# Performance work log

Measured on AMD Instinct MI355X. Metric: run time of the kernel, lower is better.

## Reference

```python
import jax, jax.numpy as jnp
import numpy as np
import math

B, T, C, H, S = 2, 2048, 1024, 16, 16
HD = C // H
EPS = 1e-5


def setup_inputs() -> dict:
    key = jax.random.key(0)
    ks = jax.random.split(key, 20)
    sc = 1.0 / math.sqrt(C)
    inp = {
        "x": jax.random.normal(ks[0], (B, T, C), jnp.float32),
        # A_log_fwd: log(arange(1..S)) repeated over dim (as in __init__)
        "A_log": jnp.log(jnp.tile(jnp.arange(1, S + 1, dtype=jnp.float32), (C, 1))),
        # Linear weights stored (in, out); apply as x @ W + b
        "Wd": jax.random.normal(ks[1], (C, C), jnp.float32) * sc,
        "bd": jnp.full((C,), -3.0, jnp.float32),
        "WB": jax.random.normal(ks[2], (C, S), jnp.float32) * sc,
        "WC": jax.random.normal(ks[3], (C, S), jnp.float32) * sc,
        "Wq": jax.random.normal(ks[4], (C, C), jnp.float32) * sc,
        "bq": jnp.zeros((C,), jnp.float32),
        "Wk": jax.random.normal(ks[5], (C, C), jnp.float32) * sc,
        "bk": jnp.zeros((C,), jnp.float32),
        "Wv": jax.random.normal(ks[6], (C, C), jnp.float32) * sc,
        "bv": jnp.zeros((C,), jnp.float32),
        "Wx": jax.random.normal(ks[7], (C, C), jnp.float32) * sc,
        "bx": jnp.zeros((C,), jnp.float32),
        "Wo": jax.random.normal(ks[8], (C, C), jnp.float32) * sc,
        "bo": jnp.zeros((C,), jnp.float32),
        "ln_g": jnp.ones((C,), jnp.float32),
        "ln_b": jnp.zeros((C,), jnp.float32),
        "temp": jnp.full((1, H, 1, 1), 0.5, jnp.float32),
    }
    return inp


def _forward(x, A_log, Wd, bd, WB, WC, Wq, bq, Wk, bk, Wv, bv, Wx, bx, Wo, bo, ln_g, ln_b, temp):
    x_base = x @ Wx + bx                      # (B,T,C)
    delta = jax.nn.softplus(x @ Wd + bd)      # (B,T,C)
    B_mat = x @ WB                            # (B,T,S)
    C_mat = x @ WC                            # (B,T,S)
    A = -jnp.exp(A_log)                       # (C,S)

    def scan_fn(h, inp):
        xb_t, d_t, B_t, C_t = inp             # (B,C),(B,C),(B,S),(B,S)
        bar_A = jnp.exp(d_t[..., None] * A)   # (B,C,S)
        h = bar_A * h + (d_t * xb_t)[..., None] * B_t[:, None, :]
        y = jnp.einsum('bcs,bs->bc', h, C_t)
        return h, y

    h0 = jnp.zeros((B, C, S), x.dtype)
    xs = (jnp.swapaxes(x_base, 0, 1), jnp.swapaxes(delta, 0, 1),
          jnp.swapaxes(B_mat, 0, 1), jnp.swapaxes(C_mat, 0, 1))
    _, ys = jax.lax.scan(scan_fn, h0, xs)
    out_fwd = jnp.swapaxes(ys, 0, 1)          # (B,T,C)

    # LayerNorm(x_base + out_fwd)
    hyb = x_base + out_fwd
    mu = hyb.mean(-1, keepdims=True)
    var = hyb.var(-1, keepdims=True)
    hybrid = (hyb - mu) * jax.lax.rsqrt(var + EPS) * ln_g + ln_b

    def heads(W, b):
        return (hybrid @ W + b).reshape(B, T, H, HD).transpose(0, 2, 1, 3)

    Q, K, V = heads(Wq, bq), heads(Wk, bk), heads(Wv, bv)
    scores = jnp.einsum('bhqd,bhkd->bhqk', Q, K) / math.sqrt(HD)
    scores = scores * jax.nn.softplus(temp)
    mask = jnp.tril(jnp.ones((T, T), bool))
    scores = jnp.where(mask[None, None], scores, -jnp.inf)
    attn = jax.nn.softmax(scores, axis=-1)
    out = jnp.einsum('bhqk,bhkd->bhqd', attn, V).transpose(0, 2, 1, 3).reshape(B, T, C)
    return out @ Wo + bo


def reference(x, A_log, Wd, bd, WB, WC, Wq, bq, Wk, bk, Wv, bv, Wx, bx, Wo, bo, ln_g, ln_b, temp):
    return _forward(x, A_log, Wd, bd, WB, WC, Wq, bq, Wk, bk, Wv, bv, Wx, bx, Wo, bo, ln_g, ln_b, temp)
```

## Files before the change

kernel.cpp:

```cpp
#include <hip/hip_runtime.h>
#include <math.h>

#define B_  2
#define T_  2048
#define C_  1024
#define H_  16
#define S_  16
#define HD_ 64
#define NCH 32
#define CHL 64

typedef short  short8  __attribute__((ext_vector_type(8)));
typedef unsigned short ushort8 __attribute__((ext_vector_type(8)));
typedef unsigned short ushort4v __attribute__((ext_vector_type(4)));
typedef float  f32x4   __attribute__((ext_vector_type(4)));

__device__ __forceinline__ float softplus_f(float v) {
    return fmaxf(v, 0.f) + log1pf(__expf(-fabsf(v)));
}

__device__ __forceinline__ unsigned short f2bf(float x) {
    unsigned u = __float_as_uint(x);
    u += 0x7fffu + ((u >> 16) & 1u);
    return (unsigned short)(u >> 16);
}

__device__ __forceinline__ void gload16(const unsigned short* g,
                                        unsigned short* l)
{
    __builtin_amdgcn_global_load_lds(
        (const __attribute__((address_space(1))) unsigned int*)g,
        (__attribute__((address_space(3))) unsigned int*)l, 16, 0, 0);
}

__global__ __launch_bounds__(256) void cast_bf16(const float* __restrict__ in,
                                                 unsigned short* __restrict__ out,
                                                 int n4)
{
    int i = blockIdx.x * 256 + threadIdx.x;
    if (i >= n4) return;
    float4 v = ((const float4*)in)[i];
    ushort4v o = {f2bf(v.x), f2bf(v.y), f2bf(v.z), f2bf(v.w)};
    ((ushort4v*)out)[i] = o;
}

__device__ __forceinline__ void wtrans_body(const float* __restrict__ W,
                                            unsigned short* __restrict__ WT,
                                            int bx, int by, int tid)
{
    __shared__ float t[32][33];
    const int n0 = bx * 32, k0 = by * 32;
    const int tx = tid & 31, ty = tid >> 5;
#pragma unroll
    for (int p = 0; p < 4; ++p)
        t[ty + p * 8][tx] = W[(size_t)(k0 + ty + p * 8) * C_ + n0 + tx];
    __syncthreads();
#pragma unroll
    for (int p = 0; p < 4; ++p)
        WT[(size_t)(n0 + ty + p * 8) * C_ + k0 + tx] = f2bf(t[tx][ty + p * 8]);
}

__global__ __launch_bounds__(256) void wtrans(const float* __restrict__ W,
                                              unsigned short* __restrict__ WT)
{
    wtrans_body(W, WT, blockIdx.x, blockIdx.y, threadIdx.x);
}

__global__ __launch_bounds__(256) void wtrans_multi(
    const float* __restrict__ Wx, const float* __restrict__ Wd,
    const float* __restrict__ Wq, const float* __restrict__ Wk,
    const float* __restrict__ Wv,
    unsigned short* __restrict__ Astack, unsigned short* __restrict__ Wqkv)
{
    const float* src;
    unsigned short* dst;
    switch (blockIdx.z) {
        case 0: src = Wx; dst = Astack; break;
        case 1: src = Wd; dst = Astack + (size_t)1024 * 1024; break;
        case 2: src = Wq; dst = Wqkv; break;
        case 3: src = Wk; dst = Wqkv + (size_t)1024 * 1024; break;
        default: src = Wv; dst = Wqkv + (size_t)2048 * 1024; break;
    }
    wtrans_body(src, dst, blockIdx.x, blockIdx.y, threadIdx.x);
}

__global__ __launch_bounds__(256) void prep_misc(
    const float* __restrict__ WB, const float* __restrict__ WC,
    const float* __restrict__ bx, const float* __restrict__ bd,
    const float* __restrict__ bq, const float* __restrict__ bk,
    const float* __restrict__ bv,
    unsigned short* __restrict__ Astack, float* __restrict__ biasPD,
    float* __restrict__ biasQKV)
{
    int gid = blockIdx.x * 256 + threadIdx.x;
    if (gid < 32768) {
        int w = gid >> 14, rem = gid & 16383;
        int s = rem >> 10, k = rem & 1023;
        const float* src = w ? WC : WB;
        Astack[(size_t)(2048 + w * 16 + s) * 1024 + k] = f2bf(src[k * 16 + s]);
    } else {
        int id = gid - 32768;
        if (id < 2176) {
            biasPD[id] = id < 1024 ? bx[id] : (id < 2048 ? bd[id - 1024] : 0.f);
        } else {
            int id2 = id - 2176;
            if (id2 < 3072)
                biasQKV[id2] = id2 < 1024 ? bq[id2]
                             : (id2 < 2048 ? bk[id2 - 1024] : bv[id2 - 2048]);
        }
    }
}

__global__ __launch_bounds__(256) void gemm_mfma(
    const unsigned short* __restrict__ A, const unsigned short* __restrict__ Bm,
    const float* __restrict__ bias,
    void* __restrict__ outv,
    int M, int N, int K, int lda)
{
    __shared__ __align__(16) unsigned short As[4][4096];
    __shared__ __align__(16) unsigned short Bs[4][4096];

    const int tid = threadIdx.x;
    const int w = tid >> 6, lane = tid & 63;
    const int lq = lane & 15, lg = lane >> 4;
    const int wm = w >> 1, wn = w & 1;
    const int mBase = blockIdx.y * 128, nBase = blockIdx.x * 128;

    const int c0 = tid, c1 = tid + 256;
    const int rA0 = ((c0 >> 6) << 4) + (c0 & 15), kO0 = ((c0 >> 4) & 3) << 3;
    const int rA1 = ((c1 >> 6) << 4) + (c1 & 15), kO1 = ((c1 >> 4) & 3) << 3;

    const int wL0 = w * 512;
    const int wL1 = 2048 + w * 512;

    f32x4 acc[4][4];
#pragma unroll
    for (int i = 0; i < 4; ++i)
#pragma unroll
        for (int j = 0; j < 4; ++j) acc[i][j] = (f32x4){0.f, 0.f, 0.f, 0.f};

    const unsigned short* ga0 = A  + (size_t)(mBase + rA0) * lda + kO0;
    const unsigned short* ga1 = A  + (size_t)(mBase + rA1) * lda + kO1;
    const unsigned short* gb0 = Bm + (size_t)(nBase + rA0) * lda + kO0;
    const unsigned short* gb1 = Bm + (size_t)(nBase + rA1) * lda + kO1;

    #define STAGE(bufv, k0v)                               \
        do {                                               \
            gload16(ga0 + (k0v), &As[bufv][wL0]);          \
            gload16(ga1 + (k0v), &As[bufv][wL1]);          \
            gload16(gb0 + (k0v), &Bs[bufv][wL0]);          \
            gload16(gb1 + (k0v), &Bs[bufv][wL1]);          \
        } while (0)
    #define COMPUTE(bufv)                                                       \
        do {                                                                    \
            short8 a[4], b[4];                                                  \
            _Pragma("unroll")                                                   \
            for (int i = 0; i < 4; ++i)                                         \
                a[i] = *(const short8*)&As[bufv][((wm * 4 + i) * 64 + lg * 16 + lq) * 8]; \
            _Pragma("unroll")                                                   \
            for (int j = 0; j < 4; ++j)                                         \
                b[j] = *(const short8*)&Bs[bufv][((wn * 4 + j) * 64 + lg * 16 + lq) * 8]; \
            _Pragma("unroll")                                                   \
            for (int i = 0; i < 4; ++i)                                         \
                _Pragma("unroll")                                               \
                for (int j = 0; j < 4; ++j)                                     \
                    acc[i][j] = __builtin_amdgcn_mfma_f32_16x16x32_bf16(        \
                        a[i], b[j], acc[i][j], 0, 0, 0);                        \
        } while (0)
    #define WAITV4() asm volatile("s_waitcnt vmcnt(4)" ::: "memory")
    #define WAITV0() asm volatile("s_waitcnt vmcnt(0)" ::: "memory")
    #define LGKM0()  asm volatile("s_waitcnt lgkmcnt(0)" ::: "memory")
    #define STEP(cbuf, kt)                                          \
        do {                                                        \
            if ((kt) + 32 < K) WAITV4(); else WAITV0();             \
            LGKM0();                                                \
            __builtin_amdgcn_s_barrier();                           \
            if ((kt) + 64 < K) STAGE(((cbuf) + 2) & 3, (kt) + 64);  \
            COMPUTE(cbuf);                                          \
        } while (0)

    STAGE(0, 0);
    STAGE(1, 32);

    for (int k0 = 0; k0 < K; k0 += 128) {
        STEP(0, k0);
        STEP(1, k0 + 32);
        STEP(2, k0 + 64);
        STEP(3, k0 + 96);
    }
    #undef STAGE
    #undef COMPUTE
    #undef WAITV4
    #undef WAITV0
    #undef LGKM0
    #undef STEP

    float* O = (float*)outv;
#pragma unroll
    for (int j = 0; j < 4; ++j) {
        int Cg = nBase + wn * 64 + j * 16 + lq;
        float bb = bias[Cg];
#pragma unroll
        for (int i = 0; i < 4; ++i) {
            int Rb = mBase + wm * 64 + i * 16 + lg * 4;
#pragma unroll
            for (int r = 0; r < 4; ++r)
                O[(size_t)(Rb + r) * N + Cg] = acc[i][j][r] + bb;
        }
    }
}

__global__ __launch_bounds__(512, 2) void gemm_projT(
    const unsigned short* __restrict__ A, const unsigned short* __restrict__ Bm,
    const float* __restrict__ bias,
    float* __restrict__ xbaseT, float* __restrict__ deltaT,
    float* __restrict__ BmT, float* __restrict__ CmT,
    int K, int lda)
{
    __shared__ __align__(16) unsigned short AS[2][2][4096];
    __shared__ __align__(16) unsigned short BS[2][2][8192];

    const int tid = threadIdx.x;
    const int w = tid >> 6, lane = tid & 63;
    const int lq = lane & 15, lg = lane >> 4;
    const int wm = w >> 2, wn = w & 3;
    const int mBase = blockIdx.y * 128, nBase = blockIdx.x * 256;

    const int rA = ((tid >> 6) << 4) | (tid & 15);
    const int kA = ((tid >> 4) & 3) << 3;
    const unsigned short* gA = A + (size_t)(mBase + rA) * lda + kA;
    const int eA = tid * 8;
    const int c0 = tid, c1 = tid + 512;
    const int rB0 = ((c0 >> 6) << 4) | (c0 & 15), kB0 = ((c0 >> 4) & 3) << 3;
    const int rB1 = ((c1 >> 6) << 4) | (c1 & 15), kB1 = ((c1 >> 4) & 3) << 3;
    const unsigned short* gB0 = Bm + (size_t)(nBase + rB0) * lda + kB0;
    const unsigned short* gB1 = Bm + (size_t)(nBase + rB1) * lda + kB1;

    f32x4 acc[4][4];
#pragma unroll
    for (int i = 0; i < 4; ++i)
#pragma unroll
        for (int j = 0; j < 4; ++j) acc[i][j] = (f32x4){0.f, 0.f, 0.f, 0.f};

    #define STG(buf_, half_, kb_)                                             \
        do {                                                                  \
            gload16(gA  + (kb_) + (half_) * 32, &AS[buf_][half_][eA]);        \
            gload16(gB0 + (kb_) + (half_) * 32, &BS[buf_][half_][c0 * 8]);    \
            gload16(gB1 + (kb_) + (half_) * 32, &BS[buf_][half_][c1 * 8]);    \
        } while (0)
    #define WAITV6() asm volatile("s_waitcnt vmcnt(6)" ::: "memory")
    #define WAITV3() asm volatile("s_waitcnt vmcnt(3)" ::: "memory")
    #define WAITV0() asm volatile("s_waitcnt vmcnt(0)" ::: "memory")

    #define PHASE(buf_, half_, STAGE_STMT, GATE_STMT)                         \
        do {                                                                  \
            short8 a_[4], b_[4];                                              \
            _Pragma("unroll")                                                 \
            for (int i = 0; i < 4; ++i)                                       \
                a_[i] = *(const short8*)&AS[buf_][half_]                      \
                    [((wm * 4 + i) * 64 + lg * 16 + lq) * 8];                 \
            _Pragma("unroll")                                                 \
            for (int j = 0; j < 4; ++j)                                       \
                b_[j] = *(const short8*)&BS[buf_][half_]                      \
                    [((wn * 4 + j) * 64 + lg * 16 + lq) * 8];                 \
            STAGE_STMT;                                                       \
            __builtin_amdgcn_s_barrier();                                     \
            asm volatile("s_waitcnt lgkmcnt(0)" ::: "memory");                \
            __builtin_amdgcn_s_setprio(1);                                    \
            _Pragma("unroll")                                                 \
            for (int i = 0; i < 4; ++i)                                       \
                _Pragma("unroll")                                             \
                for (int j = 0; j < 4; ++j)                                   \
                    acc[i][j] = __builtin_amdgcn_mfma_f32_16x16x32_bf16(      \
                        a_[i], b_[j], acc[i][j], 0, 0, 0);                    \
            __builtin_amdgcn_s_setprio(0);                                    \
            GATE_STMT;                                                        \
            __builtin_amdgcn_s_barrier();                                     \
        } while (0)

    STG(0, 0, 0);
    STG(0, 1, 0);
    STG(1, 0, 64);
    WAITV6();
    __builtin_amdgcn_s_barrier();

    const int NT = K >> 6;
    for (int kt = 0; kt < NT; ++kt) {
        const int buf = kt & 1, nbuf = buf ^ 1;
        const int kb1 = (kt + 1) << 6, kb2 = (kt + 2) << 6;
        PHASE(buf, 0, { if (kt + 1 < NT) STG(nbuf, 1, kb1); },
              { if (kt < NT - 1) WAITV6(); else WAITV3(); });
        PHASE(buf, 1, { if (kt + 2 < NT) STG(buf, 0, kb2); },
              { if (kt < NT - 2) WAITV6();
                else if (kt == NT - 2) WAITV3(); else WAITV0(); });
    }
    #undef STG
    #undef WAITV6
    #undef WAITV3
    #undef WAITV0
    #undef PHASE

#pragma unroll
    for (int i = 0; i < 4; ++i) {
        int Rb = mBase + wm * 64 + i * 16 + lg * 4;
        if (Rb >= 2080) continue;
        float bb[4];
#pragma unroll
        for (int r = 0; r < 4; ++r) bb[r] = bias[Rb + r];
#pragma unroll
        for (int j = 0; j < 4; ++j) {
            int Cg = nBase + wn * 64 + j * 16 + lq;
            int b = Cg >> 11, t = Cg & (T_ - 1);
#pragma unroll
            for (int r = 0; r < 4; ++r) {
                int R = Rb + r;
                float v = acc[i][j][r] + bb[r];
                if (Rb < 1024) {
                    xbaseT[((size_t)b * C_ + R) * T_ + t] = v;
                } else if (Rb < 2048) {
                    deltaT[((size_t)b * C_ + (R - 1024)) * T_ + t] =
                        softplus_f(v);
                } else if (Rb < 2064) {
                    BmT[((size_t)b * S_ + (R - 2048)) * T_ + t] = v;
                } else {
                    CmT[((size_t)b * S_ + (R - 2064)) * T_ + t] = v;
                }
            }
        }
    }
}

__global__ __launch_bounds__(512, 2) void gemm_mfma256(
    const unsigned short* __restrict__ A, const unsigned short* __restrict__ Bm,
    const float* __restrict__ bias,
    void* __restrict__ outv, void* __restrict__ out2,
    void* __restrict__ out3,
    int M, int N, int K, int lda)
{
    __shared__ __align__(16) unsigned short AS[2][2][8192];
    __shared__ __align__(16) unsigned short BS[2][2][8192];

    const int tid = threadIdx.x;
    const int w = tid >> 6, lane = tid & 63;
    const int lq = lane & 15, lg = lane >> 4;
    const int wm = w >> 2, wn = w & 3;
    const int mBase = blockIdx.y * 256, nBase = blockIdx.x * 256;

    const int c0 = tid, c1 = tid + 512;
    const int r0 = ((c0 >> 6) << 4) | (c0 & 15), k0l = ((c0 >> 4) & 3) << 3;
    const int r1 = ((c1 >> 6) << 4) | (c1 & 15), k1l = ((c1 >> 4) & 3) << 3;
    const unsigned short* gA0 = A  + (size_t)(mBase + r0) * lda + k0l;
    const unsigned short* gA1 = A  + (size_t)(mBase + r1) * lda + k1l;
    const unsigned short* gB0 = Bm + (size_t)(nBase + r0) * lda + k0l;
    const unsigned short* gB1 = Bm + (size_t)(nBase + r1) * lda + k1l;

    f32x4 acc[8][4];
#pragma unroll
    for (int i = 0; i < 8; ++i)
#pragma unroll
        for (int j = 0; j < 4; ++j) acc[i][j] = (f32x4){0.f, 0.f, 0.f, 0.f};

    #define STG_A(buf_, half_, kb_)                                           \
        do {                                                                  \
            gload16(gA0 + (kb_) + (half_) * 32, &AS[buf_][half_][c0 * 8]);    \
            gload16(gA1 + (kb_) + (half_) * 32, &AS[buf_][half_][c1 * 8]);    \
        } while (0)
    #define STG_B(buf_, half_, kb_)                                           \
        do {                                                                  \
            gload16(gB0 + (kb_) + (half_) * 32, &BS[buf_][half_][c0 * 8]);    \
            gload16(gB1 + (kb_) + (half_) * 32, &BS[buf_][half_][c1 * 8]);    \
        } while (0)
    #define WAITV8() asm volatile("s_waitcnt vmcnt(8)" ::: "memory")
    #define WAITV4() asm volatile("s_waitcnt vmcnt(4)" ::: "memory")
    #define WAITV0() asm volatile("s_waitcnt vmcnt(0)" ::: "memory")

    #define PHASE(buf_, half_, qi_, STAGE_STMT, GATE_STMT)                    \
        do {                                                                  \
            short8 a_[4];                                                     \
            _Pragma("unroll")                                                 \
            for (int i = 0; i < 4; ++i)                                       \
                a_[i] = *(const short8*)&AS[buf_][half_]                      \
                    [((wm * 8 + (qi_) * 4 + i) * 64 + lg * 16 + lq) * 8];     \
            if ((qi_) == 0) {                                                 \
                _Pragma("unroll")                                             \
                for (int j = 0; j < 4; ++j)                                   \
                    bfr[j] = *(const short8*)&BS[buf_][half_]                 \
                        [((wn * 4 + j) * 64 + lg * 16 + lq) * 8];             \
            }                                                                 \
            STAGE_STMT;                                                       \
            __builtin_amdgcn_s_barrier();                                     \
            asm volatile("s_waitcnt lgkmcnt(0)" ::: "memory");                \
            __builtin_amdgcn_s_setprio(1);                                    \
            _Pragma("unroll")                                                 \
            for (int i = 0; i < 4; ++i)                                       \
                _Pragma("unroll")                                             \
                for (int j = 0; j < 4; ++j)                                   \
                    acc[(qi_) * 4 + i][j] =                                   \
                        __builtin_amdgcn_mfma_f32_16x16x32_bf16(              \
                            a_[i], bfr[j], acc[(qi_) * 4 + i][j], 0, 0, 0);   \
            __builtin_amdgcn_s_setprio(0);                                    \
            GATE_STMT;                                                        \
            __builtin_amdgcn_s_barrier();                                     \
        } while (0)

    STG_A(0, 0, 0);
    STG_B(0, 0, 0);
    STG_A(0, 1, 0);
    STG_B(0, 1, 0);
    STG_A(1, 0, 64);
    STG_B(1, 0, 64);
    WAITV8();
    __builtin_amdgcn_s_barrier();

    const int NT = K >> 6;
    for (int kt = 0; kt < NT; ++kt) {
        const int buf = kt & 1, nbuf = buf ^ 1;
        const int kb1 = (kt + 1) << 6, kb2 = (kt + 2) << 6;
        short8 bfr[4];
        PHASE(buf, 0, 0, { if (kt + 1 < NT) STG_A(nbuf, 1, kb1); }, {});
        PHASE(buf, 0, 1, { if (kt + 1 < NT) STG_B(nbuf, 1, kb1); },
              { if (kt < NT - 1) WAITV8(); else WAITV0(); });
        PHASE(buf, 1, 0, { if (kt + 2 < NT) STG_A(buf, 0, kb2); }, {});
        PHASE(buf, 1, 1, { if (kt + 2 < NT) STG_B(buf, 0, kb2); },
              { if (kt < NT - 2) WAITV8();
                else if (kt == NT - 2) WAITV4(); });
    }
    #undef STG_A
    #undef STG_B
    #undef WAITV8
    #undef WAITV4
    #undef WAITV0
    #undef PHASE

    unsigned short* Qb  = (unsigned short*)outv;
    unsigned short* Kb  = (unsigned short*)out2;
    unsigned short* VTb = (unsigned short*)out3;
#pragma unroll
    for (int j = 0; j < 4; ++j) {
        int Cg = nBase + wn * 64 + j * 16 + lq;
        int reg = Cg >> 10, c = Cg & 1023;
        int h = c >> 6, hd = c & 63;
        float bb = bias[Cg];
#pragma unroll
        for (int i = 0; i < 8; ++i) {
            int Rb = mBase + wm * 128 + i * 16 + lg * 4;
#pragma unroll
            for (int r = 0; r < 4; ++r) {
                int R = Rb + r, b = R >> 11, t = R & (T_ - 1);
                unsigned short o = f2bf(acc[i][j][r] + bb);
                if (reg == 0)
                    Qb[(((size_t)(b * H_ + h) * T_ + t) * HD_) + hd] = o;
                else if (reg == 1)
                    Kb[(((size_t)(b * H_ + h) * T_ + t) * HD_) + hd] = o;
                else
                    VTb[(((size_t)(b * H_ + h) * HD_ + hd) * T_) + t] = o;
            }
        }
    }
}

__global__ __launch_bounds__(256) void scan_partial(
    const float* __restrict__ xbaseT, const float* __restrict__ deltaT,
    const float* __restrict__ BmT, const float* __restrict__ A_log,
    float4* __restrict__ Pbuf, float4* __restrict__ Lbuf)
{
    const int tid = threadIdx.x;
    const int s4 = tid & 3;
    const int cm = tid >> 2;
    const int cg = blockIdx.x & 15;
    const int k  = (blockIdx.x >> 4) & (NCH - 1);
    const int b  = blockIdx.x >> 9;
    const int c  = cg * 64 + cm;

    float a[4];
#pragma unroll
    for (int j = 0; j < 4; ++j)
        a[j] = -__expf(A_log[c * S_ + s4 * 4 + j]);

    const int tb = k * CHL;
    const float* dp = deltaT + ((size_t)b * C_ + c) * T_ + tb;
    const float* xp = xbaseT + ((size_t)b * C_ + c) * T_ + tb;
    const float* bp = BmT + ((size_t)(b * S_ + s4 * 4)) * T_ + tb;

    float L[4] = {0.f, 0.f, 0.f, 0.f};
    float sumd = 0.f;
    for (int t0 = 0; t0 < CHL; t0 += 4) {
        float4 d4 = *(const float4*)&dp[t0];
        float4 x4 = *(const float4*)&xp[t0];
        float dv[4] = {d4.x, d4.y, d4.z, d4.w};
        float xv[4] = {x4.x, x4.y, x4.z, x4.w};
        float bv[4][4];
#pragma unroll
        for (int j = 0; j < 4; ++j) {
            float4 b4 = *(const float4*)&bp[(size_t)j * T_ + t0];
            bv[j][0] = b4.x; bv[j][1] = b4.y; bv[j][2] = b4.z; bv[j][3] = b4.w;
        }
#pragma unroll
        for (int q = 0; q < 4; ++q) {
            float u = dv[q] * xv[q];
            sumd += dv[q];
#pragma unroll
            for (int j = 0; j < 4; ++j)
                L[j] = fmaf(__expf(dv[q] * a[j]), L[j], u * bv[j][q]);
        }
    }
    int gid = blockIdx.x * 256 + tid;
    float4 P4 = {__expf(a[0] * sumd), __expf(a[1] * sumd),
                 __expf(a[2] * sumd), __expf(a[3] * sumd)};
    float4 L4 = {L[0], L[1], L[2], L[3]};
    Pbuf[gid] = P4;
    Lbuf[gid] = L4;
}

__global__ __launch_bounds__(256) void scan_final(
    const float* __restrict__ xbaseT, const float* __restrict__ deltaT,
    const float* __restrict__ BmT, const float* __restrict__ CmT,
    const float* __restrict__ A_log, const float4* __restrict__ Pbuf,
    const float4* __restrict__ Lbuf, float* __restrict__ hyb)
{
    const int tid = threadIdx.x;
    const int s4 = tid & 3;
    const int cm = tid >> 2;
    const int cg = blockIdx.x & 15;
    const int k  = (blockIdx.x >> 4) & (NCH - 1);
    const int b  = blockIdx.x >> 9;
    const int c  = cg * 64 + cm;

    float h[4] = {0.f, 0.f, 0.f, 0.f};
    for (int k2 = 0; k2 < k; ++k2) {
        int gid2 = (((b * NCH + k2) << 4) + cg) * 256 + tid;
        float4 P4 = Pbuf[gid2];
        float4 L4 = Lbuf[gid2];
        h[0] = fmaf(P4.x, h[0], L4.x);
        h[1] = fmaf(P4.y, h[1], L4.y);
        h[2] = fmaf(P4.z, h[2], L4.z);
        h[3] = fmaf(P4.w, h[3], L4.w);
    }

    float a[4];
#pragma unroll
    for (int j = 0; j < 4; ++j)
        a[j] = -__expf(A_log[c * S_ + s4 * 4 + j]);

    const int tb = k * CHL;
    const float* dp = deltaT + ((size_t)b * C_ + c) * T_ + tb;
    const float* xp = xbaseT + ((size_t)b * C_ + c) * T_ + tb;
    const float* bp = BmT + ((size_t)(b * S_ + s4 * 4)) * T_ + tb;
    const float* cp = CmT + ((size_t)(b * S_ + s4 * 4)) * T_ + tb;
    float* hp = hyb + ((size_t)b * T_ + tb) * C_ + c;

    for (int t0 = 0; t0 < CHL; t0 += 4) {
        float4 d4 = *(const float4*)&dp[t0];
        float4 x4 = *(const float4*)&xp[t0];
        float dv[4] = {d4.x, d4.y, d4.z, d4.w};
        float xv[4] = {x4.x, x4.y, x4.z, x4.w};
        float bv[4][4], cv[4][4];
#pragma unroll
        for (int j = 0; j < 4; ++j) {
            float4 b4 = *(const float4*)&bp[(size_t)j * T_ + t0];
            float4 c4 = *(const float4*)&cp[(size_t)j * T_ + t0];
            bv[j][0] = b4.x; bv[j][1] = b4.y; bv[j][2] = b4.z; bv[j][3] = b4.w;
            cv[j][0] = c4.x; cv[j][1] = c4.y; cv[j][2] = c4.z; cv[j][3] = c4.w;
        }
#pragma unroll
        for (int q = 0; q < 4; ++q) {
            float u = dv[q] * xv[q];
#pragma unroll
            for (int j = 0; j < 4; ++j)
                h[j] = fmaf(__expf(dv[q] * a[j]), h[j], u * bv[j][q]);
            float y = h[0] * cv[0][q];
            y = fmaf(h[1], cv[1][q], y);
            y = fmaf(h[2], cv[2][q], y);
            y = fmaf(h[3], cv[3][q], y);
            y += __shfl_xor(y, 1, 64);
            y += __shfl_xor(y, 2, 64);
            if (s4 == 0) hp[(size_t)(t0 + q) * C_] = xv[q] + y;
        }
    }
}

__global__ __launch_bounds__(256) void layernorm_kernel(
    const float* __restrict__ in, const float* __restrict__ g,
    const float* __restrict__ beta, unsigned short* __restrict__ out)
{
    const int row = blockIdx.x;
    const float* rp = in + (size_t)row * C_;
    const int c = threadIdx.x * 4;
    float4 v = *(const float4*)&rp[c];
    float sum = v.x + v.y + v.z + v.w;
    float sq = v.x * v.x + v.y * v.y + v.z * v.z + v.w * v.w;
#pragma unroll
    for (int off = 1; off < 64; off <<= 1) {
        sum += __shfl_xor(sum, off, 64);
        sq += __shfl_xor(sq, off, 64);
    }
    __shared__ float sS[4], sQ[4];
    int wave = threadIdx.x >> 6, lane = threadIdx.x & 63;
    if (lane == 0) { sS[wave] = sum; sQ[wave] = sq; }
    __syncthreads();
    sum = sS[0] + sS[1] + sS[2] + sS[3];
    sq = sQ[0] + sQ[1] + sQ[2] + sQ[3];
    const float mu = sum * (1.f / C_);
    const float var = sq * (1.f / C_) - mu * mu;
    const float rstd = rsqrtf(var + 1e-5f);
    float4 gg = *(const float4*)&g[c];
    float4 bb = *(const float4*)&beta[c];
    ushort4v o;
    o.x = f2bf((v.x - mu) * rstd * gg.x + bb.x);
    o.y = f2bf((v.y - mu) * rstd * gg.y + bb.y);
    o.z = f2bf((v.z - mu) * rstd * gg.z + bb.z);
    o.w = f2bf((v.w - mu) * rstd * gg.w + bb.w);
    *(ushort4v*)&out[(size_t)row * C_ + c] = o;
}

#define BKT 128
#define KP  72
#define VP  136
__global__ __launch_bounds__(256) void attn_mfma(
    const unsigned short* __restrict__ Q, const unsigned short* __restrict__ K,
    const unsigned short* __restrict__ VT, const float* __restrict__ temp,
    unsigned short* __restrict__ out)
{
    __shared__ __align__(16) unsigned short Ks[BKT * KP];
    __shared__ __align__(16) unsigned short Vs[80 * VP];
    __shared__ __align__(16) unsigned short Ps[64 * VP];

    const int tid = threadIdx.x;
    const int w = tid >> 6, lane = tid & 63;
    const int lq = lane & 15, lg = lane >> 4;
    const int p  = blockIdx.x & 15;
    const int bh = blockIdx.x >> 4;
    const int b = bh >> 4, h = bh & 15;

    const float scale = softplus_f(temp[h]) * 0.125f;
    const unsigned short* Qp = Q + (size_t)bh * T_ * HD_;
    const unsigned short* Kp = K + (size_t)bh * T_ * HD_;
    const unsigned short* Vp = VT + (size_t)bh * HD_ * T_;

    {
        int r = 64 + (tid >> 4), o = (tid & 15) * 8;
        ushort8 ones = {0x3f80, 0x3f80, 0x3f80, 0x3f80,
                        0x3f80, 0x3f80, 0x3f80, 0x3f80};
        *(ushort8*)&Vs[r * VP + o] = ones;
    }

    ushort8 kreg[4], vreg[4];
    #define LOADKV(jtv)                                                        \
        do {                                                                   \
            int kb = (jtv) * BKT;                                              \
            _Pragma("unroll")                                                  \
            for (int q2 = 0; q2 < 4; ++q2) {                                   \
                int c = tid + q2 * 256;                                        \
                kreg[q2] = *(const ushort8*)&Kp[(size_t)(kb + (c >> 3)) * HD_  \
                                                + (c & 7) * 8];                \
                vreg[q2] = *(const ushort8*)&Vp[(size_t)(c >> 4) * T_ + kb     \
                                                + (c & 15) * 8];               \
            }                                                                  \
        } while (0)

    for (int half = 0; half < 2; ++half) {
        const int qi = half ? p : (31 - p);
        const int qbase = qi * 64;
        const int nT = (qbase + 64 + BKT - 1) / BKT;

        short8 qf[2];
#pragma unroll
        for (int s = 0; s < 2; ++s)
            qf[s] = *(const short8*)&Qp[(size_t)(qbase + w * 16 + lq) * HD_
                                        + s * 32 + lg * 8];
        LOADKV(0);

        float m_i[4];
        f32x4 o[5];
#pragma unroll
        for (int r = 0; r < 4; ++r) m_i[r] = -INFINITY;
#pragma unroll
        for (int j = 0; j < 5; ++j) o[j] = (f32x4){0.f, 0.f, 0.f, 0.f};

        for (int jt = 0; jt < nT; ++jt) {
            const int kbase = jt * BKT;
            const bool last = (jt == nT - 1);
            __syncthreads();
#pragma unroll
            for (int q2 = 0; q2 < 4; ++q2) {
                int c = tid + q2 * 256;
                *(ushort8*)&Ks[(c >> 3) * KP + (c & 7) * 8] = kreg[q2];
                *(ushort8*)&Vs[(c >> 4) * VP + (c & 15) * 8] = vreg[q2];
            }
            __syncthreads();
            if (jt + 1 < nT) LOADKV(jt + 1);

            f32x4 sacc[8];
#pragma unroll
            for (int j = 0; j < 8; ++j) sacc[j] = (f32x4){0.f, 0.f, 0.f, 0.f};
#pragma unroll
            for (int s = 0; s < 2; ++s) {
#pragma unroll
                for (int j = 0; j < 8; ++j) {
                    short8 kf = *(const short8*)&Ks[(j * 16 + lq) * KP
                                                    + s * 32 + lg * 8];
                    sacc[j] = __builtin_amdgcn_mfma_f32_16x16x32_bf16(
                        qf[s], kf, sacc[j], 0, 0, 0);
                }
            }

#pragma unroll
            for (int r = 0; r < 4; ++r) {
                int qrow = qbase + w * 16 + lg * 4 + r;
                float sv[8];
#pragma unroll
                for (int j = 0; j < 8; ++j) {
                    sv[j] = sacc[j][r] * scale;
                    if (last && (kbase + j * 16 + lq > qrow)) sv[j] = -INFINITY;
                }
                float mx = sv[0];
#pragma unroll
                for (int j = 1; j < 8; ++j) mx = fmaxf(mx, sv[j]);
                mx = fmaxf(mx, __shfl_xor(mx, 1, 64));
                mx = fmaxf(mx, __shfl_xor(mx, 2, 64));
                mx = fmaxf(mx, __shfl_xor(mx, 4, 64));
                mx = fmaxf(mx, __shfl_xor(mx, 8, 64));
                float mnew = fmaxf(m_i[r], mx);
                float alpha = __expf(m_i[r] - mnew);
                m_i[r] = mnew;
#pragma unroll
                for (int j = 0; j < 5; ++j) o[j][r] *= alpha;
#pragma unroll
                for (int j = 0; j < 8; ++j)
                    Ps[(w * 16 + lg * 4 + r) * VP + j * 16 + lq] =
                        f2bf(__expf(sv[j] - mnew));
            }

#pragma unroll
            for (int s2 = 0; s2 < 4; ++s2) {
                short8 pf = *(const short8*)&Ps[(w * 16 + lq) * VP
                                                + s2 * 32 + lg * 8];
#pragma unroll
                for (int j = 0; j < 5; ++j) {
                    short8 vf = *(const short8*)&Vs[(j * 16 + lq) * VP
                                                    + s2 * 32 + lg * 8];
                    o[j] = __builtin_amdgcn_mfma_f32_16x16x32_bf16(
                        pf, vf, o[j], 0, 0, 0);
                }
            }
        }

#pragma unroll
        for (int r = 0; r < 4; ++r) {
            float inv = 1.f / o[4][r];
            int qrow = qbase + w * 16 + lg * 4 + r;
#pragma unroll
            for (int j = 0; j < 4; ++j)
                out[((size_t)(b * T_ + qrow)) * C_ + h * 64 + j * 16 + lq] =
                    f2bf(o[j][r] * inv);
        }
    }
    #undef LOADKV
}

extern "C" void kernel_launch(void* const* d_in, const int* in_sizes, int n_in,
                              void* d_out, int out_size, void* d_ws, size_t ws_size,
                              hipStream_t stream)
{
    const float* x     = (const float*)d_in[0];
    const float* A_log = (const float*)d_in[1];
    const float* Wd    = (const float*)d_in[2];
    const float* bd    = (const float*)d_in[3];
    const float* WB    = (const float*)d_in[4];
    const float* WC    = (const float*)d_in[5];
    const float* Wq    = (const float*)d_in[6];
    const float* bq    = (const float*)d_in[7];
    const float* Wk    = (const float*)d_in[8];
    const float* bk    = (const float*)d_in[9];
    const float* Wv    = (const float*)d_in[10];
    const float* bv    = (const float*)d_in[11];
    const float* Wx    = (const float*)d_in[12];
    const float* bx    = (const float*)d_in[13];
    const float* Wo    = (const float*)d_in[14];
    const float* bo    = (const float*)d_in[15];
    const float* ln_g  = (const float*)d_in[16];
    const float* ln_b  = (const float*)d_in[17];
    const float* temp  = (const float*)d_in[18];

    char* wsb = (char*)d_ws;
    const size_t MB = 1024 * 1024;
    const size_t HMB = 512 * 1024;
    unsigned short* xb      = (unsigned short*)(wsb);
    float4* Pbuf            = (float4*)(wsb);
    float4* Lbuf            = (float4*)(wsb + 4 * MB);
    unsigned short* hybrid  = (unsigned short*)(wsb);
    unsigned short* Astack  = (unsigned short*)(wsb + 8 * MB);
    float* biasPD           = (float*)(wsb + 8 * MB + (size_t)2176 * 2048);
    float* biasQKV          = biasPD + 2176;
    unsigned short* WqkvT   = (unsigned short*)(wsb + 12 * MB + HMB);
    unsigned short* WoT     = (unsigned short*)(wsb + 18 * MB + HMB);
    float* deltaT           = (float*)(wsb + 18 * MB + HMB);
    float* xbaseT           = (float*)(wsb + 34 * MB + HMB);
    float* hyb              = (float*)(wsb + 50 * MB + HMB);
    float* BmT              = (float*)(wsb + 66 * MB + HMB);
    float* CmT              = BmT + (size_t)B_ * S_ * T_;
    unsigned short* Qb      = (unsigned short*)(wsb + 20 * MB + HMB);
    unsigned short* Kb      = (unsigned short*)(wsb + 28 * MB + HMB);
    unsigned short* VTb     = (unsigned short*)(wsb + 36 * MB + HMB);
    unsigned short* attnO   = (unsigned short*)(wsb + 44 * MB + HMB);

    cast_bf16<<<4096, 256, 0, stream>>>(x, xb, (B_ * T_ * C_) / 4);
    wtrans_multi<<<dim3(32, 32, 5), 256, 0, stream>>>(Wx, Wd, Wq, Wk, Wv,
                                                      Astack, WqkvT);
    prep_misc<<<149, 256, 0, stream>>>(WB, WC, bx, bd, bq, bk, bv,
                                       Astack, biasPD, biasQKV);

    gemm_projT<<<dim3(16, 17, 1), 512, 0, stream>>>(
        Astack, xb, biasPD, xbaseT, deltaT, BmT, CmT,
        1024, 1024);

    const int scanBlocks = B_ * NCH * (C_ / 64);
    scan_partial<<<scanBlocks, 256, 0, stream>>>(xbaseT, deltaT, BmT, A_log,
                                                 Pbuf, Lbuf);
    scan_final<<<scanBlocks, 256, 0, stream>>>(xbaseT, deltaT, BmT, CmT, A_log,
                                               Pbuf, Lbuf, hyb);

    layernorm_kernel<<<B_ * T_, 256, 0, stream>>>(hyb, ln_g, ln_b, hybrid);

    gemm_mfma256<<<dim3(12, 16, 1), 512, 0, stream>>>(
        hybrid, WqkvT, biasQKV, Qb, Kb, VTb,
        4096, 3072, 1024, 1024);

    attn_mfma<<<B_ * H_ * 16, 256, 0, stream>>>(Qb, Kb, VTb, temp, attnO);

    wtrans<<<dim3(32, 32), 256, 0, stream>>>(Wo, WoT);
    gemm_mfma<<<dim3(8, 32, 1), 256, 0, stream>>>(
        attnO, WoT, bo, d_out,
        4096, 1024, 1024, 1024);
}
```

Measured before the change: 453.5 us.

## Use more, shorter scan chunks and prefetch next-step operands in scan kernels

```diff
diff --git a/kernel.cpp b/kernel.cpp
--- a/kernel.cpp
+++ b/kernel.cpp
@@ -7,8 +7,8 @@
 #define H_  16
 #define S_  16
 #define HD_ 64
-#define NCH 32
-#define CHL 64
+#define NCH 64
+#define CHL 32
 
 typedef short  short8  __attribute__((ext_vector_type(8)));
 typedef unsigned short ushort8 __attribute__((ext_vector_type(8)));
@@ -469,7 +469,7 @@
     const int cm = tid >> 2;
     const int cg = blockIdx.x & 15;
     const int k  = (blockIdx.x >> 4) & (NCH - 1);
-    const int b  = blockIdx.x >> 9;
+    const int b  = blockIdx.x >> 10;
     const int c  = cg * 64 + cm;
 
     float a[4];
@@ -484,16 +484,29 @@
 
     float L[4] = {0.f, 0.f, 0.f, 0.f};
     float sumd = 0.f;
+
+    float4 d4 = *(const float4*)&dp[0];
+    float4 x4 = *(const float4*)&xp[0];
+    float4 b4[4];
+#pragma unroll
+    for (int j = 0; j < 4; ++j) b4[j] = *(const float4*)&bp[(size_t)j * T_];
+
     for (int t0 = 0; t0 < CHL; t0 += 4) {
-        float4 d4 = *(const float4*)&dp[t0];
-        float4 x4 = *(const float4*)&xp[t0];
+        const int tn = (t0 + 4 < CHL) ? t0 + 4 : t0;
+        float4 d4n = *(const float4*)&dp[tn];
+        float4 x4n = *(const float4*)&xp[tn];
+        float4 b4n[4];
+#pragma unroll
+        for (int j = 0; j < 4; ++j)
+            b4n[j] = *(const float4*)&bp[(size_t)j * T_ + tn];
+
         float dv[4] = {d4.x, d4.y, d4.z, d4.w};
         float xv[4] = {x4.x, x4.y, x4.z, x4.w};
         float bv[4][4];
 #pragma unroll
         for (int j = 0; j < 4; ++j) {
-            float4 b4 = *(const float4*)&bp[(size_t)j * T_ + t0];
-            bv[j][0] = b4.x; bv[j][1] = b4.y; bv[j][2] = b4.z; bv[j][3] = b4.w;
+            bv[j][0] = b4[j].x; bv[j][1] = b4[j].y;
+            bv[j][2] = b4[j].z; bv[j][3] = b4[j].w;
         }
 #pragma unroll
         for (int q = 0; q < 4; ++q) {
@@ -503,6 +516,9 @@
             for (int j = 0; j < 4; ++j)
                 L[j] = fmaf(__expf(dv[q] * a[j]), L[j], u * bv[j][q]);
         }
+        d4 = d4n; x4 = x4n;
+#pragma unroll
+        for (int j = 0; j < 4; ++j) b4[j] = b4n[j];
     }
     int gid = blockIdx.x * 256 + tid;
     float4 P4 = {__expf(a[0] * sumd), __expf(a[1] * sumd),
@@ -523,14 +539,22 @@
     const int cm = tid >> 2;
     const int cg = blockIdx.x & 15;
     const int k  = (blockIdx.x >> 4) & (NCH - 1);
-    const int b  = blockIdx.x >> 9;
+    const int b  = blockIdx.x >> 10;
     const int c  = cg * 64 + cm;
 
     float h[4] = {0.f, 0.f, 0.f, 0.f};
-    for (int k2 = 0; k2 < k; ++k2) {
-        int gid2 = (((b * NCH + k2) << 4) + cg) * 256 + tid;
-        float4 P4 = Pbuf[gid2];
-        float4 L4 = Lbuf[gid2];
+    if (k > 0) {
+        const size_t g0 = (size_t)(((b * NCH) << 4) + cg) * 256 + tid;
+        float4 P4 = Pbuf[g0], L4 = Lbuf[g0];
+        for (int k2 = 1; k2 < k; ++k2) {
+            size_t gn = g0 + (size_t)k2 * 4096;
+            float4 P4n = Pbuf[gn], L4n = Lbuf[gn];
+            h[0] = fmaf(P4.x, h[0], L4.x);
+            h[1] = fmaf(P4.y, h[1], L4.y);
+            h[2] = fmaf(P4.z, h[2], L4.z);
+            h[3] = fmaf(P4.w, h[3], L4.w);
+            P4 = P4n; L4 = L4n;
+        }
         h[0] = fmaf(P4.x, h[0], L4.x);
         h[1] = fmaf(P4.y, h[1], L4.y);
         h[2] = fmaf(P4.z, h[2], L4.z);
@@ -549,18 +573,35 @@
     const float* cp = CmT + ((size_t)(b * S_ + s4 * 4)) * T_ + tb;
     float* hp = hyb + ((size_t)b * T_ + tb) * C_ + c;
 
+    float4 d4 = *(const float4*)&dp[0];
+    float4 x4 = *(const float4*)&xp[0];
+    float4 b4[4], c4[4];
+#pragma unroll
+    for (int j = 0; j < 4; ++j) {
+        b4[j] = *(const float4*)&bp[(size_t)j * T_];
+        c4[j] = *(const float4*)&cp[(size_t)j * T_];
+    }
+
     for (int t0 = 0; t0 < CHL; t0 += 4) {
-        float4 d4 = *(const float4*)&dp[t0];
-        float4 x4 = *(const float4*)&xp[t0];
+        const int tn = (t0 + 4 < CHL) ? t0 + 4 : t0;
+        float4 d4n = *(const float4*)&dp[tn];
+        float4 x4n = *(const float4*)&xp[tn];
+        float4 b4n[4], c4n[4];
+#pragma unroll
+        for (int j = 0; j < 4; ++j) {
+            b4n[j] = *(const float4*)&bp[(size_t)j * T_ + tn];
+            c4n[j] = *(const float4*)&cp[(size_t)j * T_ + tn];
+        }
+
         float dv[4] = {d4.x, d4.y, d4.z, d4.w};
         float xv[4] = {x4.x, x4.y, x4.z, x4.w};
         float bv[4][4], cv[4][4];
 #pragma unroll
         for (int j = 0; j < 4; ++j) {
-            float4 b4 = *(const float4*)&bp[(size_t)j * T_ + t0];
-            float4 c4 = *(const float4*)&cp[(size_t)j * T_ + t0];
-            bv[j][0] = b4.x; bv[j][1] = b4.y; bv[j][2] = b4.z; bv[j][3] = b4.w;
-            cv[j][0] = c4.x; cv[j][1] = c4.y; cv[j][2] = c4.z; cv[j][3] = c4.w;
+            bv[j][0] = b4[j].x; bv[j][1] = b4[j].y;
+            bv[j][2] = b4[j].z; bv[j][3] = b4[j].w;
+            cv[j][0] = c4[j].x; cv[j][1] = c4[j].y;
+            cv[j][2] = c4[j].z; cv[j][3] = c4[j].w;
         }
 #pragma unroll
         for (int q = 0; q < 4; ++q) {
@@ -576,6 +617,9 @@
             y += __shfl_xor(y, 2, 64);
             if (s4 == 0) hp[(size_t)(t0 + q) * C_] = xv[q] + y;
         }
+        d4 = d4n; x4 = x4n;
+#pragma unroll
+        for (int j = 0; j < 4; ++j) { b4[j] = b4n[j]; c4[j] = c4n[j]; }
     }
 }
 
@@ -787,7 +831,7 @@
     const size_t HMB = 512 * 1024;
     unsigned short* xb      = (unsigned short*)(wsb);
     float4* Pbuf            = (float4*)(wsb);
-    float4* Lbuf            = (float4*)(wsb + 4 * MB);
+    float4* Lbuf            = (float4*)d_out;
     unsigned short* hybrid  = (unsigned short*)(wsb);
     unsigned short* Astack  = (unsigned short*)(wsb + 8 * MB);
     float* biasPD           = (float*)(wsb + 8 * MB + (size_t)2176 * 2048);
```

Result: slower. 471.5 us (+4.0%).
